# Optimization experiments

Measured on AMD Instinct MI355X. Metric: run time of the kernel, lower is better.

The kernel has to match this reference:

```python
import jax, jax.numpy as jnp
import numpy as np

N_NODES = 20000
N_REL = 200
DIM = 128
N_EDGES = 200000
N_TIMES = 8


def setup_inputs() -> dict:
    key = jax.random.key(0)
    ks = jax.random.split(key, 12)
    s = 1.0 / np.sqrt(DIM)
    return {
        "edge_index": jax.random.randint(ks[0], (2, N_EDGES), 0, N_NODES),
        "edge_type": jax.random.randint(ks[1], (N_EDGES,), 0, N_REL),
        "edge_time": jax.random.randint(ks[2], (N_EDGES,), 0, N_TIMES),
        "edge_weight": jax.random.uniform(ks[3], (N_EDGES,), dtype=jnp.float32),
        "node_emb": jax.random.normal(ks[4], (N_NODES, DIM), dtype=jnp.float32),
        "rel_emb": jax.random.normal(ks[5], (N_REL, DIM), dtype=jnp.float32),
        "W_enc": jax.random.normal(ks[6], (DIM, DIM), dtype=jnp.float32) * s,
        "Wz": jax.random.normal(ks[7], (DIM, DIM), dtype=jnp.float32) * s,
        "Uz": jax.random.normal(ks[8], (DIM, DIM), dtype=jnp.float32) * s,
        "Wh": jax.random.normal(ks[9], (DIM, DIM), dtype=jnp.float32) * s,
        "Uh": jax.random.normal(ks[10], (DIM, DIM), dtype=jnp.float32) * s,
        "bz": jnp.zeros((DIM,), dtype=jnp.float32),
        "bh": jnp.zeros((DIM,), dtype=jnp.float32),
        "num_times": N_TIMES,
    }


def reference(edge_index, edge_type, edge_time, edge_weight,
              node_emb, rel_emb, W_enc, Wz, Uz, Wh, Uh, bz, bh, num_times):
    # TemporalEncoder.forward: loop over sorted unique timestamps; per-step
    # masked-edge GNN encode (R-GCN lite) then gated SSM cell; state detached.
    src, dst = edge_index[0], edge_index[1]
    rel_e = rel_emb[edge_type]          # [E, D] gather (constant across steps)
    src_e = node_emb[src]               # [E, D]
    n_nodes = node_emb.shape[0]

    def step(state, t):
        m = (edge_time == t).astype(edge_weight.dtype)       # [E]
        msg = src_e * rel_e * (edge_weight * m)[:, None]     # [E, D]
        agg = jax.ops.segment_sum(msg, dst, num_segments=n_nodes)  # [N, D]
        h = jnp.tanh(agg @ W_enc)                            # base_encoder output
        z = jax.nn.sigmoid(h @ Wz + state @ Uz + bz)
        cand = jnp.tanh(h @ Wh + state @ Uh + bh)
        new_state = (1.0 - z) * state + z * cand             # ssm.cell
        return jax.lax.stop_gradient(new_state), new_state   # state.detach()

    state0 = jnp.zeros_like(node_emb)
    _, outs = jax.lax.scan(step, state0, jnp.arange(num_times))
    return outs[-1]  # last_out, shape [N, D]
```

## Files before the change

### kernel.cpp

```cpp
#include <hip/hip_runtime.h>

#define N_NODES 20000
#define N_REL 200
#define N_EDGES 200000
#define DIM 128
#define T_STEPS 8
#define N_TILES (N_NODES / 16)
#define KEYS (N_NODES * T_STEPS)
#define SCAN_N (KEYS + 1)
#define SCAN_BLKS ((SCAN_N + 1023) / 1024)

typedef short short8 __attribute__((ext_vector_type(8)));
typedef float f32x4 __attribute__((ext_vector_type(4)));

static __device__ __forceinline__ unsigned short f2bf(float f) {
  union { float f; unsigned u; } v; v.f = f;
  unsigned r = v.u + 0x7fffu + ((v.u >> 16) & 1u);
  return (unsigned short)(r >> 16);
}
static __device__ __forceinline__ unsigned cvt_pk_bf16(float lo, float hi) {
  unsigned r;
  asm("v_cvt_pk_bf16_f32 %0, %1, %2" : "=v"(r) : "v"(lo), "v"(hi));
  return r;
}
static __device__ __forceinline__ float fast_tanh(float x) {
  float e = __expf(2.f * x);
  return 1.f - 2.f / (e + 1.f);
}
static __device__ __forceinline__ float fast_sig(float x) {
  return 1.f / (1.f + __expf(-x));
}

__global__ void repack5(const float* __restrict__ w0,
                        const float* __restrict__ w1,
                        const float* __restrict__ w2,
                        const float* __restrict__ w3,
                        const float* __restrict__ w4,
                        unsigned short* __restrict__ pack) {
  int i = blockIdx.x * blockDim.x + threadIdx.x;
  if (i >= 5 * 16384) return;
  int m = i >> 14, r = i & 16383;
  int j = r & 7, lane = (r >> 3) & 63, ks = (r >> 9) & 3, nt = (r >> 11) & 7;
  int n = nt * 16 + (lane & 15);
  int k = ks * 32 + (lane >> 4) * 8 + j;
  const float* w = (m == 0) ? w0 : (m == 1) ? w1 : (m == 2) ? w2
                 : (m == 3) ? w3 : w4;
  pack[i] = f2bf(w[k * DIM + n]);
}

__global__ void hist_k(const int* __restrict__ dst, const int* __restrict__ etime,
                       int* __restrict__ counts) {
  int i = blockIdx.x * blockDim.x + threadIdx.x;
  if (i >= N_EDGES) return;
  atomicAdd(&counts[dst[i] * T_STEPS + etime[i]], 1);
}

__global__ void scan1_k(const int* __restrict__ counts,
                        int* __restrict__ base, int* __restrict__ bsum) {
  __shared__ int ls[256];
  int tid = threadIdx.x;
  int i0 = blockIdx.x * 1024 + tid * 4;
  int v[4], ts = 0;
#pragma unroll
  for (int r = 0; r < 4; r++) {
    v[r] = (i0 + r < SCAN_N) ? counts[i0 + r] : 0;
    ts += v[r];
  }
  ls[tid] = ts; __syncthreads();
#pragma unroll
  for (int off = 1; off < 256; off <<= 1) {
    int x = (tid >= off) ? ls[tid - off] : 0;
    __syncthreads(); ls[tid] += x; __syncthreads();
  }
  int run = ls[tid] - ts;
  if (tid == 255) bsum[blockIdx.x] = ls[255];
#pragma unroll
  for (int r = 0; r < 4; r++) {
    if (i0 + r < SCAN_N) base[i0 + r] = run;
    run += v[r];
  }
}

__global__ void scan2_k(int* __restrict__ bsum) {
  __shared__ int ls[256];
  int tid = threadIdx.x;
  int v = (tid < SCAN_BLKS) ? bsum[tid] : 0;
  ls[tid] = v; __syncthreads();
#pragma unroll
  for (int off = 1; off < 256; off <<= 1) {
    int x = (tid >= off) ? ls[tid - off] : 0;
    __syncthreads(); ls[tid] += x; __syncthreads();
  }
  if (tid < SCAN_BLKS) bsum[tid] = ls[tid] - v;
}

__global__ void scan3_k(int* __restrict__ base, const int* __restrict__ bsum) {
  int i = blockIdx.x * blockDim.x + threadIdx.x;
  if (i < SCAN_N) base[i] += bsum[i >> 10];
}

__global__ void fill_k(const int* __restrict__ src, const int* __restrict__ dst,
                       const int* __restrict__ etype, const int* __restrict__ etime,
                       const float* __restrict__ ew,
                       const int* __restrict__ base, int* __restrict__ cursor,
                       uint2* __restrict__ ep2) {
  int i = blockIdx.x * blockDim.x + threadIdx.x;
  if (i >= N_EDGES) return;
  int key = dst[i] * T_STEPS + etime[i];
  int pos = base[key] + atomicAdd(&cursor[key], 1);
  uint2 e;
  e.x = (unsigned)src[i] | ((unsigned)etype[i] << 15);
  e.y = __float_as_uint(ew[i]);
  ep2[pos] = e;
}

__global__ void gather_k(const int* __restrict__ base,
                         const uint2* __restrict__ ep2,
                         const float* __restrict__ nemb,
                         const float* __restrict__ remb,
                         unsigned short* __restrict__ aggb) {
  int lane = threadIdx.x & 63;
  int node = (blockIdx.x * blockDim.x + threadIdx.x) >> 6;
  const int* b = base + node * T_STEPS;
  int i = b[0];
#pragma unroll
  for (int tt = 0; tt < T_STEPS; tt++) {
    int e1 = b[tt + 1];
    float ax = 0.f, ay = 0.f;
    for (; i < e1; i++) {
      uint2 e = ep2[i];
      float w = __uint_as_float(e.y);
      int s = e.x & 0x7fff, rt = e.x >> 15;
      float2 sv = ((const float2*)(nemb + (size_t)s * DIM))[lane];
      float2 rv = ((const float2*)(remb + (size_t)rt * DIM))[lane];
      ax += sv.x * rv.x * w;
      ay += sv.y * rv.y * w;
    }
    ((unsigned*)(aggb + ((size_t)tt * N_NODES + node) * DIM))[lane] =
        cvt_pk_bf16(ax, ay);
  }
}

__launch_bounds__(512, 4)
__global__ void fused_recur(const unsigned short* __restrict__ aggb,
                            const unsigned short* __restrict__ pack,
                            const float* __restrict__ bz,
                            const float* __restrict__ bh,
                            float* __restrict__ out) {
  __shared__ unsigned short Hb[2][16 * 136];
  __shared__ unsigned short Sb[2][16 * 136];
  int lane = threadIdx.x & 63;
  int nt = threadIdx.x >> 6;
  int tile = blockIdx.x;
  int q = lane >> 4, l15 = lane & 15;
  int row0 = tile * 16;

  unsigned hpk[T_STEPS][2];
  {
    short8 wenc[4];
#pragma unroll
    for (int ks = 0; ks < 4; ks++) {
      wenc[ks] = *(const short8*)(pack + ((nt * 4 + ks) * 64 + lane) * 8);
      asm volatile("" : "+v"(wenc[ks]));
    }
#pragma unroll
    for (int t = 0; t < T_STEPS; t++) {
      f32x4 acch = (f32x4){0.f, 0.f, 0.f, 0.f};
#pragma unroll
      for (int ks = 0; ks < 4; ks++) {
        short8 aA = *(const short8*)(aggb +
            ((size_t)t * N_NODES + row0 + l15) * DIM + ks * 32 + q * 8);
        acch = __builtin_amdgcn_mfma_f32_16x16x32_bf16(aA, wenc[ks], acch, 0, 0, 0);
      }
      hpk[t][0] = cvt_pk_bf16(fast_tanh(acch[0]), fast_tanh(acch[1]));
      hpk[t][1] = cvt_pk_bf16(fast_tanh(acch[2]), fast_tanh(acch[3]));
    }
  }

  short8 wz[4], uz[4], wh[4], uh[4];
#pragma unroll
  for (int ks = 0; ks < 4; ks++) {
    int fo = ((nt * 4 + ks) * 64 + lane) * 8;
    wz[ks] = *(const short8*)(pack + 16384 * 1 + fo);
    uz[ks] = *(const short8*)(pack + 16384 * 2 + fo);
    wh[ks] = *(const short8*)(pack + 16384 * 3 + fo);
    uh[ks] = *(const short8*)(pack + 16384 * 4 + fo);
    asm volatile("" : "+v"(wz[ks]));
    asm volatile("" : "+v"(uz[ks]));
    asm volatile("" : "+v"(wh[ks]));
    asm volatile("" : "+v"(uh[ks]));
  }
  float bzv = bz[nt * 16 + l15];
  float bhv = bh[nt * 16 + l15];

  f32x4 stC = (f32x4){0.f, 0.f, 0.f, 0.f};
  int c = nt * 16 + l15;

#pragma unroll
  for (int t = 0; t < T_STEPS; t++) {
    unsigned short* hB = Hb[t & 1];
    unsigned short* sB = Sb[t & 1];
    unsigned s01 = cvt_pk_bf16(stC[0], stC[1]);
    unsigned s23 = cvt_pk_bf16(stC[2], stC[3]);
    hB[(q * 4 + 0) * 136 + c] = (unsigned short)hpk[t][0];
    hB[(q * 4 + 1) * 136 + c] = (unsigned short)(hpk[t][0] >> 16);
    hB[(q * 4 + 2) * 136 + c] = (unsigned short)hpk[t][1];
    hB[(q * 4 + 3) * 136 + c] = (unsigned short)(hpk[t][1] >> 16);
    sB[(q * 4 + 0) * 136 + c] = (unsigned short)s01;
    sB[(q * 4 + 1) * 136 + c] = (unsigned short)(s01 >> 16);
    sB[(q * 4 + 2) * 136 + c] = (unsigned short)s23;
    sB[(q * 4 + 3) * 136 + c] = (unsigned short)(s23 >> 16);
    __syncthreads();

    f32x4 accz = (f32x4){bzv, bzv, bzv, bzv};
    f32x4 accc = (f32x4){bhv, bhv, bhv, bhv};
#pragma unroll
    for (int ks = 0; ks < 4; ks++) {
      short8 hA = *(const short8*)&hB[l15 * 136 + ks * 32 + q * 8];
      short8 sA = *(const short8*)&sB[l15 * 136 + ks * 32 + q * 8];
      accz = __builtin_amdgcn_mfma_f32_16x16x32_bf16(hA, wz[ks], accz, 0, 0, 0);
      accz = __builtin_amdgcn_mfma_f32_16x16x32_bf16(sA, uz[ks], accz, 0, 0, 0);
      accc = __builtin_amdgcn_mfma_f32_16x16x32_bf16(hA, wh[ks], accc, 0, 0, 0);
      accc = __builtin_amdgcn_mfma_f32_16x16x32_bf16(sA, uh[ks], accc, 0, 0, 0);
    }
#pragma unroll
    for (int r = 0; r < 4; r++) {
      float z = fast_sig(accz[r]);
      float cc = fast_tanh(accc[r]);
      stC[r] = (1.f - z) * stC[r] + z * cc;
    }
  }

#pragma unroll
  for (int r = 0; r < 4; r++)
    out[(size_t)(row0 + q * 4 + r) * DIM + nt * 16 + l15] = stC[r];
}

extern "C" void kernel_launch(void* const* d_in, const int* in_sizes, int n_in,
                              void* d_out, int out_size, void* d_ws, size_t ws_size,
                              hipStream_t stream) {
  const int* eidx  = (const int*)d_in[0];
  const int* src   = eidx;
  const int* dst   = eidx + N_EDGES;
  const int* etype = (const int*)d_in[1];
  const int* etime = (const int*)d_in[2];
  const float* ew   = (const float*)d_in[3];
  const float* nemb = (const float*)d_in[4];
  const float* remb = (const float*)d_in[5];
  const float* Wenc = (const float*)d_in[6];
  const float* Wz   = (const float*)d_in[7];
  const float* Uz   = (const float*)d_in[8];
  const float* Wh   = (const float*)d_in[9];
  const float* Uh   = (const float*)d_in[10];
  const float* bz   = (const float*)d_in[11];
  const float* bh   = (const float*)d_in[12];

  unsigned short* aggb = (unsigned short*)d_ws;
  int* counts = (int*)(aggb + (size_t)T_STEPS * N_NODES * DIM);
  int* cursor = counts + SCAN_N;
  int* bsum   = cursor + KEYS;
  int* base   = bsum + 256;
  uint2* ep2  = (uint2*)(base + ((SCAN_N + 1) & ~1));
  unsigned short* pack = (unsigned short*)(ep2 + N_EDGES);
  float* outp = (float*)d_out;

  hipMemsetAsync(counts, 0, (size_t)(SCAN_N + KEYS) * sizeof(int), stream);
  repack5<<<(5 * 16384 + 255) / 256, 256, 0, stream>>>(Wenc, Wz, Uz, Wh, Uh, pack);
  hist_k<<<(N_EDGES + 255) / 256, 256, 0, stream>>>(dst, etime, counts);
  scan1_k<<<SCAN_BLKS, 256, 0, stream>>>(counts, base, bsum);
  scan2_k<<<1, 256, 0, stream>>>(bsum);
  scan3_k<<<(SCAN_N + 255) / 256, 256, 0, stream>>>(base, bsum);
  fill_k<<<(N_EDGES + 255) / 256, 256, 0, stream>>>(src, dst, etype, etime, ew,
                                                    base, cursor, ep2);
  gather_k<<<N_NODES / 4, 256, 0, stream>>>(base, ep2, nemb, remb, aggb);
  fused_recur<<<N_TILES, 512, 0, stream>>>(aggb, pack, bz, bh, outp);
}
```

Baseline: 225.9 us.

## Process 32 rows per block in fused recurrence to amortize weight loads

The fused recurrent kernel now handles two 16-row tiles per block instead of one. This halves the number of blocks, each of which loads the five packed weight matrices into registers, and it halves the barriers per row processed. In exchange it holds twice the hidden and state registers, lowers the occupancy bound from 4 to 3 blocks, and leaves 625 blocks, which may fill the GPU less evenly.

Result: slower. 253.0 us (+12.0%).

```diff
diff --git a/kernel.cpp b/kernel.cpp
--- a/kernel.cpp
+++ b/kernel.cpp
@@ -5,7 +5,8 @@
 #define N_EDGES 200000
 #define DIM 128
 #define T_STEPS 8
-#define N_TILES (N_NODES / 16)
+#define ROWS_BLK 32
+#define N_TILES32 (N_NODES / ROWS_BLK)
 #define KEYS (N_NODES * T_STEPS)
 #define SCAN_N (KEYS + 1)
 #define SCAN_BLKS ((SCAN_N + 1023) / 1024)
@@ -141,21 +142,21 @@
   }
 }
 
-__launch_bounds__(512, 4)
+__launch_bounds__(512, 3)
 __global__ void fused_recur(const unsigned short* __restrict__ aggb,
                             const unsigned short* __restrict__ pack,
                             const float* __restrict__ bz,
                             const float* __restrict__ bh,
                             float* __restrict__ out) {
-  __shared__ unsigned short Hb[2][16 * 136];
-  __shared__ unsigned short Sb[2][16 * 136];
+  __shared__ unsigned short Hb[2][ROWS_BLK * 136];
+  __shared__ unsigned short Sb[2][ROWS_BLK * 136];
   int lane = threadIdx.x & 63;
   int nt = threadIdx.x >> 6;
-  int tile = blockIdx.x;
   int q = lane >> 4, l15 = lane & 15;
-  int row0 = tile * 16;
-
-  unsigned hpk[T_STEPS][2];
+  int row0 = blockIdx.x * ROWS_BLK;
+  int c = nt * 16 + l15;
+
+  unsigned hpk[2][T_STEPS][2];
   {
     short8 wenc[4];
 #pragma unroll
@@ -164,16 +165,19 @@
       asm volatile("" : "+v"(wenc[ks]));
     }
 #pragma unroll
-    for (int t = 0; t < T_STEPS; t++) {
-      f32x4 acch = (f32x4){0.f, 0.f, 0.f, 0.f};
-#pragma unroll
-      for (int ks = 0; ks < 4; ks++) {
-        short8 aA = *(const short8*)(aggb +
-            ((size_t)t * N_NODES + row0 + l15) * DIM + ks * 32 + q * 8);
-        acch = __builtin_amdgcn_mfma_f32_16x16x32_bf16(aA, wenc[ks], acch, 0, 0, 0);
-      }
-      hpk[t][0] = cvt_pk_bf16(fast_tanh(acch[0]), fast_tanh(acch[1]));
-      hpk[t][1] = cvt_pk_bf16(fast_tanh(acch[2]), fast_tanh(acch[3]));
+    for (int rt = 0; rt < 2; rt++) {
+#pragma unroll
+      for (int t = 0; t < T_STEPS; t++) {
+        f32x4 acch = (f32x4){0.f, 0.f, 0.f, 0.f};
+#pragma unroll
+        for (int ks = 0; ks < 4; ks++) {
+          short8 aA = *(const short8*)(aggb +
+              ((size_t)t * N_NODES + row0 + rt * 16 + l15) * DIM + ks * 32 + q * 8);
+          acch = __builtin_amdgcn_mfma_f32_16x16x32_bf16(aA, wenc[ks], acch, 0, 0, 0);
+        }
+        hpk[rt][t][0] = cvt_pk_bf16(fast_tanh(acch[0]), fast_tanh(acch[1]));
+        hpk[rt][t][1] = cvt_pk_bf16(fast_tanh(acch[2]), fast_tanh(acch[3]));
+      }
     }
   }
 
@@ -190,50 +194,65 @@
     asm volatile("" : "+v"(wh[ks]));
     asm volatile("" : "+v"(uh[ks]));
   }
-  float bzv = bz[nt * 16 + l15];
-  float bhv = bh[nt * 16 + l15];
-
-  f32x4 stC = (f32x4){0.f, 0.f, 0.f, 0.f};
-  int c = nt * 16 + l15;
+  float bzv = bz[c];
+  float bhv = bh[c];
+
+  f32x4 stC[2];
+  stC[0] = (f32x4){0.f, 0.f, 0.f, 0.f};
+  stC[1] = (f32x4){0.f, 0.f, 0.f, 0.f};
 
 #pragma unroll
   for (int t = 0; t < T_STEPS; t++) {
     unsigned short* hB = Hb[t & 1];
     unsigned short* sB = Sb[t & 1];
-    unsigned s01 = cvt_pk_bf16(stC[0], stC[1]);
-    unsigned s23 = cvt_pk_bf16(stC[2], stC[3]);
-    hB[(q * 4 + 0) * 136 + c] = (unsigned short)hpk[t][0];
-    hB[(q * 4 + 1) * 136 + c] = (unsigned short)(hpk[t][0] >> 16);
-    hB[(q * 4 + 2) * 136 + c] = (unsigned short)hpk[t][1];
-    hB[(q * 4 + 3) * 136 + c] = (unsigned short)(hpk[t][1] >> 16);
-    sB[(q * 4 + 0) * 136 + c] = (unsigned short)s01;
-    sB[(q * 4 + 1) * 136 + c] = (unsigned short)(s01 >> 16);
-    sB[(q * 4 + 2) * 136 + c] = (unsigned short)s23;
-    sB[(q * 4 + 3) * 136 + c] = (unsigned short)(s23 >> 16);
+#pragma unroll
+    for (int rt = 0; rt < 2; rt++) {
+      unsigned s01 = cvt_pk_bf16(stC[rt][0], stC[rt][1]);
+      unsigned s23 = cvt_pk_bf16(stC[rt][2], stC[rt][3]);
+      int rbase = (rt * 16 + q * 4) * 136 + c;
+      hB[rbase + 0 * 136] = (unsigned short)hpk[rt][t][0];
+      hB[rbase + 1 * 136] = (unsigned short)(hpk[rt][t][0] >> 16);
+      hB[rbase + 2 * 136] = (unsigned short)hpk[rt][t][1];
+      hB[rbase + 3 * 136] = (unsigned short)(hpk[rt][t][1] >> 16);
+      sB[rbase + 0 * 136] = (unsigned short)s01;
+      sB[rbase + 1 * 136] = (unsigned short)(s01 >> 16);
+      sB[rbase + 2 * 136] = (unsigned short)s23;
+      sB[rbase + 3 * 136] = (unsigned short)(s23 >> 16);
+    }
     __syncthreads();
 
-    f32x4 accz = (f32x4){bzv, bzv, bzv, bzv};
-    f32x4 accc = (f32x4){bhv, bhv, bhv, bhv};
-#pragma unroll
-    for (int ks = 0; ks < 4; ks++) {
-      short8 hA = *(const short8*)&hB[l15 * 136 + ks * 32 + q * 8];
-      short8 sA = *(const short8*)&sB[l15 * 136 + ks * 32 + q * 8];
-      accz = __builtin_amdgcn_mfma_f32_16x16x32_bf16(hA, wz[ks], accz, 0, 0, 0);
-      accz = __builtin_amdgcn_mfma_f32_16x16x32_bf16(sA, uz[ks], accz, 0, 0, 0);
-      accc = __builtin_amdgcn_mfma_f32_16x16x32_bf16(hA, wh[ks], accc, 0, 0, 0);
-      accc = __builtin_amdgcn_mfma_f32_16x16x32_bf16(sA, uh[ks], accc, 0, 0, 0);
-    }
-#pragma unroll
-    for (int r = 0; r < 4; r++) {
-      float z = fast_sig(accz[r]);
-      float cc = fast_tanh(accc[r]);
-      stC[r] = (1.f - z) * stC[r] + z * cc;
-    }
-  }
-
-#pragma unroll
-  for (int r = 0; r < 4; r++)
-    out[(size_t)(row0 + q * 4 + r) * DIM + nt * 16 + l15] = stC[r];
+#pragma unroll
+    for (int rt = 0; rt < 2; rt++) {
+      int rb = (rt * 16 + l15) * 136 + q * 8;
+      short8 hA[4], sA[4];
+#pragma unroll
+      for (int ks = 0; ks < 4; ks++) {
+        hA[ks] = *(const short8*)&hB[rb + ks * 32];
+        sA[ks] = *(const short8*)&sB[rb + ks * 32];
+      }
+      f32x4 accz = (f32x4){bzv, bzv, bzv, bzv};
+      f32x4 accc = (f32x4){bhv, bhv, bhv, bhv};
+#pragma unroll
+      for (int ks = 0; ks < 4; ks++) {
+        accz = __builtin_amdgcn_mfma_f32_16x16x32_bf16(hA[ks], wz[ks], accz, 0, 0, 0);
+        accz = __builtin_amdgcn_mfma_f32_16x16x32_bf16(sA[ks], uz[ks], accz, 0, 0, 0);
+        accc = __builtin_amdgcn_mfma_f32_16x16x32_bf16(hA[ks], wh[ks], accc, 0, 0, 0);
+        accc = __builtin_amdgcn_mfma_f32_16x16x32_bf16(sA[ks], uh[ks], accc, 0, 0, 0);
+      }
+#pragma unroll
+      for (int r = 0; r < 4; r++) {
+        float z = fast_sig(accz[r]);
+        float cc = fast_tanh(accc[r]);
+        stC[rt][r] = (1.f - z) * stC[rt][r] + z * cc;
+      }
+    }
+  }
+
+#pragma unroll
+  for (int rt = 0; rt < 2; rt++)
+#pragma unroll
+    for (int r = 0; r < 4; r++)
+      out[(size_t)(row0 + rt * 16 + q * 4 + r) * DIM + c] = stC[rt][r];
 }
 
 extern "C" void kernel_launch(void* const* d_in, const int* in_sizes, int n_in,
@@ -273,5 +292,5 @@
   fill_k<<<(N_EDGES + 255) / 256, 256, 0, stream>>>(src, dst, etype, etime, ew,
                                                     base, cursor, ep2);
   gather_k<<<N_NODES / 4, 256, 0, stream>>>(base, ep2, nemb, remb, aggb);
-  fused_recur<<<N_TILES, 512, 0, stream>>>(aggb, pack, bz, bh, outp);
-}
+  fused_recur<<<N_TILES32, 512, 0, stream>>>(aggb, pack, bz, bh, outp);
+}
```

## Fuse edge gather into recurrent kernel via LDS and fold scan fixup into consumers

Applied to the files above, without the earlier changes.

Removes the separate gather kernel and the global bf16 aggregate buffer. Each 512-thread block now gathers messages for its 16 nodes across all time steps straight into shared memory before the MFMA recurrence. The scan3 fixup kernel is also dropped, and each consumer adds the block offset from bsum itself. This cuts a global write and re-read of the per-step aggregates plus two launches, but each fused block now uses more LDS and must finish the irregular gather before any MFMA work starts, which may lower occupancy and overlap.

Result: faster. 213.1 us (-5.7%).

```diff
diff --git a/kernel.cpp b/kernel.cpp
--- a/kernel.cpp
+++ b/kernel.cpp
@@ -94,82 +94,77 @@
   if (tid < SCAN_BLKS) bsum[tid] = ls[tid] - v;
 }
 
-__global__ void scan3_k(int* __restrict__ base, const int* __restrict__ bsum) {
-  int i = blockIdx.x * blockDim.x + threadIdx.x;
-  if (i < SCAN_N) base[i] += bsum[i >> 10];
-}
-
 __global__ void fill_k(const int* __restrict__ src, const int* __restrict__ dst,
                        const int* __restrict__ etype, const int* __restrict__ etime,
                        const float* __restrict__ ew,
-                       const int* __restrict__ base, int* __restrict__ cursor,
-                       uint2* __restrict__ ep2) {
+                       const int* __restrict__ base, const int* __restrict__ bsum,
+                       int* __restrict__ cursor, uint2* __restrict__ ep2) {
   int i = blockIdx.x * blockDim.x + threadIdx.x;
   if (i >= N_EDGES) return;
   int key = dst[i] * T_STEPS + etime[i];
-  int pos = base[key] + atomicAdd(&cursor[key], 1);
+  int pos = base[key] + bsum[key >> 10] + atomicAdd(&cursor[key], 1);
   uint2 e;
   e.x = (unsigned)src[i] | ((unsigned)etype[i] << 15);
   e.y = __float_as_uint(ew[i]);
   ep2[pos] = e;
 }
 
-__global__ void gather_k(const int* __restrict__ base,
-                         const uint2* __restrict__ ep2,
-                         const float* __restrict__ nemb,
-                         const float* __restrict__ remb,
-                         unsigned short* __restrict__ aggb) {
-  int lane = threadIdx.x & 63;
-  int node = (blockIdx.x * blockDim.x + threadIdx.x) >> 6;
-  const int* b = base + node * T_STEPS;
-  int i = b[0];
-#pragma unroll
-  for (int tt = 0; tt < T_STEPS; tt++) {
-    int e1 = b[tt + 1];
-    float ax = 0.f, ay = 0.f;
-    for (; i < e1; i++) {
-      uint2 e = ep2[i];
-      float w = __uint_as_float(e.y);
-      int s = e.x & 0x7fff, rt = e.x >> 15;
-      float2 sv = ((const float2*)(nemb + (size_t)s * DIM))[lane];
-      float2 rv = ((const float2*)(remb + (size_t)rt * DIM))[lane];
-      ax += sv.x * rv.x * w;
-      ay += sv.y * rv.y * w;
-    }
-    ((unsigned*)(aggb + ((size_t)tt * N_NODES + node) * DIM))[lane] =
-        cvt_pk_bf16(ax, ay);
-  }
-}
-
 __launch_bounds__(512, 4)
-__global__ void fused_recur(const unsigned short* __restrict__ aggb,
+__global__ void fused_recur(const int* __restrict__ base,
+                            const int* __restrict__ bsum,
+                            const uint2* __restrict__ ep2,
+                            const float* __restrict__ nemb,
+                            const float* __restrict__ remb,
                             const unsigned short* __restrict__ pack,
                             const float* __restrict__ bz,
                             const float* __restrict__ bh,
                             float* __restrict__ out) {
+  __shared__ unsigned short aggL[T_STEPS * 16 * 136];
   __shared__ unsigned short Hb[2][16 * 136];
   __shared__ unsigned short Sb[2][16 * 136];
   int lane = threadIdx.x & 63;
   int nt = threadIdx.x >> 6;
-  int tile = blockIdx.x;
   int q = lane >> 4, l15 = lane & 15;
-  int row0 = tile * 16;
+  int row0 = blockIdx.x * 16;
+  int c = nt * 16 + l15;
+
+#pragma unroll
+  for (int ln = 0; ln < 2; ln++) {
+    int nl = nt * 2 + ln;
+    int kb = (row0 + nl) * T_STEPS;
+    int prev = base[kb] + bsum[kb >> 10];
+#pragma unroll
+    for (int tt = 0; tt < T_STEPS; tt++) {
+      int kn = kb + tt + 1;
+      int e1 = base[kn] + bsum[kn >> 10];
+      float ax = 0.f, ay = 0.f;
+      for (int i = prev; i < e1; i++) {
+        uint2 e = ep2[i];
+        float w = __uint_as_float(e.y);
+        int s = e.x & 0x7fff, rt = e.x >> 15;
+        float2 sv = ((const float2*)(nemb + (size_t)s * DIM))[lane];
+        float2 rv = ((const float2*)(remb + (size_t)rt * DIM))[lane];
+        ax += sv.x * rv.x * w;
+        ay += sv.y * rv.y * w;
+      }
+      prev = e1;
+      ((unsigned*)&aggL[(tt * 16 + nl) * 136])[lane] = cvt_pk_bf16(ax, ay);
+    }
+  }
+  __syncthreads();
 
   unsigned hpk[T_STEPS][2];
   {
     short8 wenc[4];
 #pragma unroll
-    for (int ks = 0; ks < 4; ks++) {
+    for (int ks = 0; ks < 4; ks++)
       wenc[ks] = *(const short8*)(pack + ((nt * 4 + ks) * 64 + lane) * 8);
-      asm volatile("" : "+v"(wenc[ks]));
-    }
 #pragma unroll
     for (int t = 0; t < T_STEPS; t++) {
       f32x4 acch = (f32x4){0.f, 0.f, 0.f, 0.f};
 #pragma unroll
       for (int ks = 0; ks < 4; ks++) {
-        short8 aA = *(const short8*)(aggb +
-            ((size_t)t * N_NODES + row0 + l15) * DIM + ks * 32 + q * 8);
+        short8 aA = *(const short8*)&aggL[(t * 16 + l15) * 136 + ks * 32 + q * 8];
         acch = __builtin_amdgcn_mfma_f32_16x16x32_bf16(aA, wenc[ks], acch, 0, 0, 0);
       }
       hpk[t][0] = cvt_pk_bf16(fast_tanh(acch[0]), fast_tanh(acch[1]));
@@ -185,16 +180,11 @@
     uz[ks] = *(const short8*)(pack + 16384 * 2 + fo);
     wh[ks] = *(const short8*)(pack + 16384 * 3 + fo);
     uh[ks] = *(const short8*)(pack + 16384 * 4 + fo);
-    asm volatile("" : "+v"(wz[ks]));
-    asm volatile("" : "+v"(uz[ks]));
-    asm volatile("" : "+v"(wh[ks]));
-    asm volatile("" : "+v"(uh[ks]));
-  }
-  float bzv = bz[nt * 16 + l15];
-  float bhv = bh[nt * 16 + l15];
+  }
+  float bzv = bz[c];
+  float bhv = bh[c];
 
   f32x4 stC = (f32x4){0.f, 0.f, 0.f, 0.f};
-  int c = nt * 16 + l15;
 
 #pragma unroll
   for (int t = 0; t < T_STEPS; t++) {
@@ -233,7 +223,7 @@
 
 #pragma unroll
   for (int r = 0; r < 4; r++)
-    out[(size_t)(row0 + q * 4 + r) * DIM + nt * 16 + l15] = stC[r];
+    out[(size_t)(row0 + q * 4 + r) * DIM + c] = stC[r];
 }
 
 extern "C" void kernel_launch(void* const* d_in, const int* in_sizes, int n_in,
@@ -255,8 +245,7 @@
   const float* bz   = (const float*)d_in[11];
   const float* bh   = (const float*)d_in[12];
 
-  unsigned short* aggb = (unsigned short*)d_ws;
-  int* counts = (int*)(aggb + (size_t)T_STEPS * N_NODES * DIM);
+  int* counts = (int*)d_ws;
   int* cursor = counts + SCAN_N;
   int* bsum   = cursor + KEYS;
   int* base   = bsum + 256;
@@ -269,9 +258,8 @@
   hist_k<<<(N_EDGES + 255) / 256, 256, 0, stream>>>(dst, etime, counts);
   scan1_k<<<SCAN_BLKS, 256, 0, stream>>>(counts, base, bsum);
   scan2_k<<<1, 256, 0, stream>>>(bsum);
-  scan3_k<<<(SCAN_N + 255) / 256, 256, 0, stream>>>(base, bsum);
   fill_k<<<(N_EDGES + 255) / 256, 256, 0, stream>>>(src, dst, etype, etime, ew,
-                                                    base, cursor, ep2);
-  gather_k<<<N_NODES / 4, 256, 0, stream>>>(base, ep2, nemb, remb, aggb);
-  fused_recur<<<N_TILES, 512, 0, stream>>>(aggb, pack, bz, bh, outp);
-}
+                                                    base, bsum, cursor, ep2);
+  fused_recur<<<N_TILES, 512, 0, stream>>>(base, bsum, ep2, nemb, remb,
+                                           pack, bz, bh, outp);
+}
```
